# Optimization experiments

Measured on AMD Instinct MI355X. Metric: run time of the kernel, lower is better.

## Reference

```python
import jax, jax.numpy as jnp
import numpy as np

N = 50000   # nodes
E = 800000  # edges (before self loops)
F = 128     # in_dim
H = 4       # heads
C = 32      # hidden_dim per head
HC = H * C  # 128 == F
L = 3       # n_layers
G = 64      # graphs in batch
OUT = 64    # out_dim
NEG_SLOPE = 0.2


def setup_inputs() -> dict:
    key = jax.random.key(0)
    ks = jax.random.split(key, 12)
    s = 0.1
    x = jax.random.normal(ks[0], (N, F), jnp.float32)
    src = jax.random.randint(ks[1], (E,), 0, N, dtype=jnp.int32)
    dst = jax.random.randint(ks[2], (E,), 0, N, dtype=jnp.int32)
    # even split into G graphs so no graph is empty (segment_max safe)
    batch = (jnp.arange(N, dtype=jnp.int32) * G // N).astype(jnp.int32)
    Ws = jax.random.normal(ks[3], (L, HC, HC), jnp.float32) * s       # layer0 in=F=HC
    att_src = jax.random.normal(ks[4], (L, H, C), jnp.float32) * s
    att_dst = jax.random.normal(ks[5], (L, H, C), jnp.float32) * s
    conv_b = jnp.zeros((L, HC), jnp.float32)
    gate_W = jax.random.normal(ks[6], (L + 1, HC, 1), jnp.float32) * s
    gate_b = jnp.zeros((L + 1,), jnp.float32)
    lin_W = jax.random.normal(ks[7], (L + 1, HC, OUT), jnp.float32) * s
    lin_b = jnp.zeros((L + 1, OUT), jnp.float32)
    h_weights = jnp.ones((L + 1,), jnp.float32) / (L + 1)
    h0 = jax.random.normal(ks[8], (1,), jnp.float32)
    beta = jax.random.normal(ks[9], (OUT,), jnp.float32) * s
    pool_w = jnp.ones((3,), jnp.float32) / 3.0
    return dict(x=x, src=src, dst=dst, batch=batch, Ws=Ws, att_src=att_src,
                att_dst=att_dst, conv_b=conv_b, gate_W=gate_W, gate_b=gate_b,
                lin_W=lin_W, lin_b=lin_b, h_weights=h_weights, h0=h0,
                beta=beta, pool_w=pool_w)


def _seg_softmax(e, idx, n):
    # numerically stable softmax within segments
    m = jax.ops.segment_max(e, idx, num_segments=n)
    m = jnp.where(jnp.isfinite(m), m, 0.0)
    ex = jnp.exp(e - m[idx])
    s = jax.ops.segment_sum(ex, idx, num_segments=n)
    return ex / (s[idx] + 1e-16)


def _gat_layer(x, src, dst, W, a_src, a_dst, b):
    h = (x @ W).reshape(N, H, C)               # [N,H,C]
    al_s = jnp.sum(h * a_src, axis=-1)         # [N,H]
    al_d = jnp.sum(h * a_dst, axis=-1)         # [N,H]
    e = jax.nn.leaky_relu(al_s[src] + al_d[dst], NEG_SLOPE)  # [E+N,H]
    alpha = _seg_softmax(e, dst, N)            # softmax over incoming edges
    msg = h[src] * alpha[..., None]            # [E+N,H,C]
    out = jax.ops.segment_sum(msg, dst, num_segments=N)
    return out.reshape(N, HC) + b


def _pool_block(x, gw, gb, pool_w, batch, counts):
    gate = jax.nn.sigmoid(x @ gw + gb)[:, 0]          # [N]
    a = _seg_softmax(gate, batch, G)                  # per-graph attention
    p_att = jax.ops.segment_sum(a[:, None] * x, batch, num_segments=G)
    p_mean = jax.ops.segment_sum(x, batch, num_segments=G) / counts[:, None]
    p_max = jax.ops.segment_max(x, batch, num_segments=G)
    return pool_w[0] * p_att + pool_w[1] * p_mean + pool_w[2] * p_max


def reference(x, src, dst, batch, Ws, att_src, att_dst, conv_b, gate_W,
              gate_b, lin_W, lin_b, h_weights, h0, beta, pool_w):
    loops = jnp.arange(N, dtype=src.dtype)
    src_sl = jnp.concatenate([src, loops])
    dst_sl = jnp.concatenate([dst, loops])
    counts = jax.ops.segment_sum(jnp.ones((N,), x.dtype), batch, num_segments=G)
    out = jnp.zeros((G, OUT), x.dtype)
    for i in range(L):
        p = _pool_block(x, gate_W[i], gate_b[i], pool_w, batch, counts)
        out = out + h_weights[i] * (p @ lin_W[i] + lin_b[i])
        x = _gat_layer(x, src_sl, dst_sl, Ws[i], att_src[i], att_dst[i], conv_b[i])
        if i != L - 1:
            x = jax.nn.relu(x)
    p = _pool_block(x, gate_W[L], gate_b[L], pool_w, batch, counts)
    out = out + h_weights[L] * (p @ lin_W[L] + lin_b[L])
    risk_score = out @ beta + h0[0]   # [G]
    return risk_score
```

## Files before the change

kernel.cpp:

```cpp
#include <hip/hip_runtime.h>
#include <hip/hip_fp16.h>
#include <math.h>

#define N_NODES 50000
#define N_EDGES 800000
#define HC 128
#define NH 4
#define NG 64
#define NOUT 64
#define NLAYERS 3
#define POOL_CHUNKS 16
#define PREPW_BLOCKS (NLAYERS * HC * HC / 256)
#define NBKT ((N_NODES + 127) / 128)
#define PB_BLOCKS ((N_EDGES + 4095) / 4096)
#define GEMM_BLOCKS ((N_NODES + 15) / 16)
#define POOL2_BLOCKS (NG * POOL_CHUNKS / 2)
#define AGG_BLOCKS ((N_NODES + 3) / 4)
#define XT_STRIDE 136
#define ZREG_FLOATS ((NLAYERS + 1) * NG * HC * 2 + (NLAYERS + 1) * NG)
#define ZREG_BLOCKS ((ZREG_FLOATS / 4 + 255) / 256)
#define PMAX_BLOCKS ((NLAYERS + 1) * NG * HC / 4 / 256)
#define LOG2E 1.44269504f

typedef _Float16 v4h __attribute__((ext_vector_type(4)));
typedef float v4f __attribute__((ext_vector_type(4)));
typedef float v2f __attribute__((ext_vector_type(2)));

typedef unsigned char hh_t;

__device__ __forceinline__ void graph_range(int g, int* start, int* end) {
    *start = (int)(((long long)g * N_NODES + NG - 1) / NG);
    *end   = (int)(((long long)(g + 1) * N_NODES + NG - 1) / NG);
}

__device__ __forceinline__ float atomicMaxFloat(float* addr, float val) {
    if (val >= 0.f)
        return __int_as_float(atomicMax((int*)addr, __float_as_int(val)));
    else
        return __uint_as_float(atomicMin((unsigned int*)addr, __float_as_uint(val)));
}

__device__ __forceinline__ v2f hh_decode2(unsigned int packed) {
    return __builtin_amdgcn_cvt_pk_f32_fp8((int)packed, false);
}


template<bool F32>
__device__ __forceinline__ void gemm_body(
        int b, const void* xin, const _Float16* __restrict__ Wt,
        const float* __restrict__ a_src, const float* __restrict__ a_dst,
        hh_t* __restrict__ hh, float* __restrict__ al_s, float* __restrict__ al_d,
        __half* __restrict__ xh_out, const float* __restrict__ gw,
        const float* __restrict__ gbp, float* __restrict__ gate) {
    __shared__ __align__(16) _Float16 xt[16][XT_STRIDE];
    int t = threadIdx.x;
    int w = t >> 6;
    int l = t & 63;
    int n0 = b * 16;
    if constexpr (F32) {
        const float4* xg = (const float4*)((const float*)xin + (size_t)n0 * HC);
        float4 v0 = xg[t];
        float4 v1 = xg[t + 256];
        float4 gwv = ((const float4*)gw)[t & 31];
        float p0 = v0.x * gwv.x + v0.y * gwv.y + v0.z * gwv.z + v0.w * gwv.w;
        float p1 = v1.x * gwv.x + v1.y * gwv.y + v1.z * gwv.z + v1.w * gwv.w;
#pragma unroll
        for (int mk = 16; mk >= 1; mk >>= 1) {
            p0 += __shfl_xor(p0, mk);
            p1 += __shfl_xor(p1, mk);
        }
        if ((t & 31) == 0) {
            int r = t >> 5;
            float sg0 = 1.f / (1.f + __expf(-(p0 + gbp[0])));
            float sg1 = 1.f / (1.f + __expf(-(p1 + gbp[0])));
            gate[n0 + r]     = __expf(sg0);
            gate[n0 + 8 + r] = __expf(sg1);
        }
        __half2 h00 = __floats2half2_rn(v0.x, v0.y);
        __half2 h01 = __floats2half2_rn(v0.z, v0.w);
        __half2 h10 = __floats2half2_rn(v1.x, v1.y);
        __half2 h11 = __floats2half2_rn(v1.z, v1.w);
        uint2 pa, pb;
        pa.x = *(const uint*)&h00; pa.y = *(const uint*)&h01;
        pb.x = *(const uint*)&h10; pb.y = *(const uint*)&h11;
        int row = t >> 5, colh = (t & 31) * 4;
        *(uint2*)&xt[row][colh] = pa;
        *(uint2*)&xt[row + 8][colh] = pb;
        ((uint2*)xh_out)[(size_t)n0 * (HC / 4) + t]       = pa;
        ((uint2*)xh_out)[(size_t)n0 * (HC / 4) + t + 256] = pb;
    } else {
        uint4 v = ((const uint4*)((const __half*)xin + (size_t)n0 * HC))[t];
        *(uint4*)&xt[t >> 4][(t & 15) * 8] = v;
    }
    __syncthreads();
    int m = l & 15;
    int kg = (l >> 4) * 4;
    v4h a[8];
#pragma unroll
    for (int ks = 0; ks < 8; ks++)
        a[ks] = *(const v4h*)&xt[m][kg + ks * 16];
    __syncthreads();
    const _Float16* bp0 = Wt + (uint)(w * 32 + m) * HC + kg;
    const _Float16* bp1 = bp0 + 16 * HC;
    v4f acc0 = {0.f, 0.f, 0.f, 0.f}, acc1 = {0.f, 0.f, 0.f, 0.f};
#pragma unroll
    for (int ks = 0; ks < 8; ks++) {
        v4h b0 = *(const v4h*)(bp0 + ks * 16);
        v4h b1 = *(const v4h*)(bp1 + ks * 16);
        acc0 = __builtin_amdgcn_mfma_f32_16x16x16f16(a[ks], b0, acc0, 0, 0, 0);
        acc1 = __builtin_amdgcn_mfma_f32_16x16x16f16(a[ks], b1, acc1, 0, 0, 0);
    }
    int d0 = w * 32 + m;
    float as0 = a_src[d0] * LOG2E,      ad0 = a_dst[d0] * LOG2E;
    float as1 = a_src[d0 + 16] * LOG2E, ad1 = a_dst[d0 + 16] * LOG2E;
    int rloc = (l >> 4) * 4;
    unsigned char* xt8 = (unsigned char*)&xt[0][0];
#pragma unroll
    for (int r = 0; r < 4; r++) {
        int n = n0 + rloc + r;
        int q0 = __builtin_amdgcn_cvt_pk_fp8_f32(acc0[r], acc0[r], 0, false);
        int q1 = __builtin_amdgcn_cvt_pk_fp8_f32(acc1[r], acc1[r], 0, false);
        xt8[(rloc + r) * 136 + d0]      = (unsigned char)(q0 & 0xFF);
        xt8[(rloc + r) * 136 + d0 + 16] = (unsigned char)(q1 & 0xFF);
        float vs = acc0[r] * as0 + acc1[r] * as1;
        float vd = acc0[r] * ad0 + acc1[r] * ad1;
#pragma unroll
        for (int mk = 8; mk >= 1; mk >>= 1) {
            vs += __shfl_xor(vs, mk);
            vd += __shfl_xor(vd, mk);
        }
        if ((l & 15) == 0) {
            al_s[(uint)(n * NH + w)] = vs;
            al_d[(uint)(n * NH + w)] = vd;
        }
    }
    __syncthreads();
    uint2 v = *(const uint2*)&xt8[(t >> 4) * 136 + (t & 15) * 8];
    ((uint2*)hh)[(size_t)n0 * 16 + t] = v;
}

__device__ __forceinline__ void pool_body(
        int b, const __half* __restrict__ x, const float* __restrict__ gate,
        float* __restrict__ p_att, float* __restrict__ p_sum,
        float* __restrict__ p_max, float* __restrict__ wsum) {
    int c = b * 2 + (threadIdx.x >> 7);
    int g = c >> 4;
    int chunk = c & 15;
    int d = threadIdx.x & 127;
    int start, end; graph_range(g, &start, &end);
    int cnt = end - start;
    int cstart = start + (cnt * chunk) / POOL_CHUNKS;
    int cend   = start + (cnt * (chunk + 1)) / POOL_CHUNKS;
    float aat = 0.f, asu = 0.f, amx = -INFINITY, ws = 0.f;
    int n = cstart;
    for (; n + 4 <= cend; n += 4) {
        float w0 = gate[n],     w1 = gate[n + 1];
        float w2 = gate[n + 2], w3 = gate[n + 3];
        float x0 = __half2float(x[(uint)((n + 0) * HC + d)]);
        float x1 = __half2float(x[(uint)((n + 1) * HC + d)]);
        float x2 = __half2float(x[(uint)((n + 2) * HC + d)]);
        float x3 = __half2float(x[(uint)((n + 3) * HC + d)]);
        aat = fmaf(w0, x0, aat); aat = fmaf(w1, x1, aat);
        aat = fmaf(w2, x2, aat); aat = fmaf(w3, x3, aat);
        asu += (x0 + x1) + (x2 + x3);
        amx = fmaxf(amx, fmaxf(fmaxf(x0, x1), fmaxf(x2, x3)));
        ws += (w0 + w1) + (w2 + w3);
    }
    for (; n < cend; n++) {
        float w = gate[n];
        float xv = __half2float(x[(uint)(n * HC + d)]);
        aat = fmaf(w, xv, aat);
        asu += xv;
        amx = fmaxf(amx, xv);
        ws += w;
    }
    atomicAdd(&p_att[g * HC + d], aat);
    atomicAdd(&p_sum[g * HC + d], asu);
    atomicMaxFloat(&p_max[g * HC + d], amx);
    if (d == 0) atomicAdd(&wsum[g], ws);
}

__device__ __forceinline__ void scat2_body(
        int bkt, const int* __restrict__ part, const int* __restrict__ bkttot,
        int* __restrict__ rowptr, int* __restrict__ csr_src) {
    __shared__ int degs[128];
    __shared__ int curs[128];
    __shared__ int red[256];
    __shared__ int w0tot;
    int t = threadIdx.x;
    int a = 0;
    for (int i = t; i < NBKT; i += 256)
        if (i < bkt) a += bkttot[i];
    red[t] = a;
    __syncthreads();
    for (int o = 128; o > 0; o >>= 1) {
        if (t < o) red[t] += red[t + o];
        __syncthreads();
    }
    int estart = red[0];
    int eend = estart + bkttot[bkt];
    int nstart = bkt << 7;
    int nend = nstart + 128; if (nend > N_NODES) nend = N_NODES;
    int nloc = nend - nstart;
    if (t < 128) degs[t] = 0;
    __syncthreads();
    for (int e = estart + t; e < eend; e += 256)
        atomicAdd(&degs[(part[e] >> 16) & 127], 1);
    __syncthreads();
    int v = 0, inc = 0;
    if (t < 128) {
        v = degs[t];
        inc = v;
#pragma unroll
        for (int off = 1; off < 64; off <<= 1) {
            int u = __shfl_up(inc, off);
            if ((t & 63) >= off) inc += u;
        }
    }
    if (t == 63) w0tot = inc;
    __syncthreads();
    if (t < 128) {
        int excl = inc - v + ((t >= 64) ? w0tot : 0);
        int rp = estart + excl;
        curs[t] = rp;
        if (t < nloc) rowptr[nstart + t] = rp;
    }
    __syncthreads();
    for (int e = estart + t; e < eend; e += 256) {
        int p = part[e];
        int pos = atomicAdd(&curs[(p >> 16) & 127], 1);
        csr_src[pos] = p & 0xFFFF;
    }
}

__device__ __forceinline__ void agg_body(
        int b, const hh_t* __restrict__ hh, const float* __restrict__ al_s,
        const float* __restrict__ al_d, const int* __restrict__ rowptr,
        const int* __restrict__ csr_src, const float* __restrict__ conv_b,
        __half* __restrict__ xout, int do_relu,
        const float* __restrict__ gw, const float* __restrict__ gbp,
        float* __restrict__ gate) {
    int n = b * 4 + (threadIdx.x >> 6);
    if (n >= N_NODES) return;
    int l = threadIdx.x & 63;
    int head = l >> 4;
    int le = l & 15;
    float ad = al_d[(uint)(n * NH + head)];
    const unsigned short* hhp = (const unsigned short*)hh;
    float e0 = al_s[(uint)(n * NH + head)] + ad;
    e0 = fmaxf(e0, 0.2f * e0);
    float s_uni = exp2f(e0);
    v2f vself = hh_decode2(hhp[(uint)(n * 64 + l)]);
    float ax = s_uni * vself[0], ay = s_uni * vself[1];
    int jb = rowptr[n], je = rowptr[n + 1];
    float s_part = 0.f;
    for (int j = jb; j < je; j += 16) {
        int rem = je - j;
        bool act = le < rem;
        int my_s = csr_src[j + (act ? le : 0)];
        float aa = al_s[(uint)(my_s * NH + head)];
        float e = aa + ad;
        e = fmaxf(e, 0.2f * e);
        float ex = act ? exp2f(e) : 0.f;
        s_part += ex;
        int exb = __float_as_int(ex);
        unsigned int vv[16];
#pragma unroll
        for (int u = 0; u < 16; u++) {
            int ssu = __builtin_amdgcn_readlane(my_s, u);
            vv[u] = hhp[((size_t)(uint)ssu << 6) + l];
        }
#define AGG_SLOT(U) {                                                        \
            float exu = __int_as_float(                                      \
                __builtin_amdgcn_ds_swizzle(exb, 16 + 32 * (U)));            \
            v2f vf = hh_decode2(vv[U]);                                      \
            ax = fmaf(exu, vf[0], ax);                                       \
            ay = fmaf(exu, vf[1], ay);                                       \
        }
        AGG_SLOT(0)  AGG_SLOT(1)  AGG_SLOT(2)  AGG_SLOT(3)
        AGG_SLOT(4)  AGG_SLOT(5)  AGG_SLOT(6)  AGG_SLOT(7)
        AGG_SLOT(8)  AGG_SLOT(9)  AGG_SLOT(10) AGG_SLOT(11)
        AGG_SLOT(12) AGG_SLOT(13) AGG_SLOT(14) AGG_SLOT(15)
#undef AGG_SLOT
    }
    s_part += __shfl_xor(s_part, 1);
    s_part += __shfl_xor(s_part, 2);
    s_part += __shfl_xor(s_part, 4);
    s_part += __shfl_xor(s_part, 8);
    float s = s_part + s_uni;
    float inv = 1.f / (s + 1e-16f);
    float2 cb = ((const float2*)conv_b)[l];
    float r0 = fmaf(ax, inv, cb.x);
    float r1 = fmaf(ay, inv, cb.y);
    if (do_relu) { r0 = fmaxf(r0, 0.f); r1 = fmaxf(r1, 0.f); }
    ((__half2*)xout)[(uint)(n * 64 + l)] = __floats2half2_rn(r0, r1);
    float2 gwv = ((const float2*)gw)[l];
    float gv = r0 * gwv.x + r1 * gwv.y;
#pragma unroll
    for (int m = 32; m >= 1; m >>= 1) gv += __shfl_xor(gv, m);
    if (l == 0) {
        float sg = 1.f / (1.f + __expf(-(gv + gbp[0])));
        gate[n] = __expf(sg);
    }
}


__global__ __launch_bounds__(256) void k_prep(
        const float* __restrict__ Ws, _Float16* __restrict__ Wt,
        const int* __restrict__ dst, int* __restrict__ bh,
        float* __restrict__ zreg, uint* __restrict__ pmaxw,
        int* __restrict__ rowptr) {
    int b = blockIdx.x;
    int t = threadIdx.x;
    if (b == 0 && t == 0) rowptr[N_NODES] = N_EDGES;
    if (b < PREPW_BLOCKS) {
        int e = b * 256 + t;
        int layer = e >> 14; int r = e & 16383; int k = r >> 7; int d = r & 127;
        Wt[layer * 16384 + d * 128 + k] = (_Float16)Ws[layer * 16384 + k * 128 + d];
    } else if (b < PREPW_BLOCKS + PB_BLOCKS) {
        int pb = b - PREPW_BLOCKS;
        __shared__ int cnt[NBKT];
        for (int i = t; i < NBKT; i += 256) cnt[i] = 0;
        __syncthreads();
        int base = pb * 4096;
#pragma unroll
        for (int k = 0; k < 16; k++) {
            int e = base + t + 256 * k;
            if (e < N_EDGES) atomicAdd(&cnt[dst[e] >> 7], 1);
        }
        __syncthreads();
        for (int i = t; i < NBKT; i += 256) bh[i * PB_BLOCKS + pb] = cnt[i];
    } else {
        int zb = b - PREPW_BLOCKS - PB_BLOCKS;
        if (zb < ZREG_BLOCKS) {
            int i = zb * 256 + t;
            if (i < ZREG_FLOATS / 4)
                ((float4*)zreg)[i] = make_float4(0.f, 0.f, 0.f, 0.f);
        } else {
            int i = (zb - ZREG_BLOCKS) * 256 + t;
            uint4 f; f.x = f.y = f.z = f.w = 0xFFFFFFFFu;
            ((uint4*)pmaxw)[i] = f;
        }
    }
}

__global__ __launch_bounds__(256) void k_scan_bh(int* __restrict__ bh,
                                                 int* __restrict__ bkttot) {
    __shared__ int tmp[256];
    int bkt = blockIdx.x, t = threadIdx.x;
    int v = (t < PB_BLOCKS) ? bh[bkt * PB_BLOCKS + t] : 0;
    tmp[t] = v;
    __syncthreads();
    for (int off = 1; off < 256; off <<= 1) {
        int u = (t >= off) ? tmp[t - off] : 0;
        __syncthreads();
        tmp[t] += u;
        __syncthreads();
    }
    if (t < PB_BLOCKS) bh[bkt * PB_BLOCKS + t] = tmp[t] - v;
    if (t == 255) bkttot[bkt] = tmp[255];
}

__global__ __launch_bounds__(256) void k_part(
        const int* __restrict__ src, const int* __restrict__ dst,
        const int* __restrict__ bkttot, const int* __restrict__ bh,
        int* __restrict__ part) {
    __shared__ int curs[NBKT];
    __shared__ int scan[512];
    int blk = blockIdx.x, t = threadIdx.x;
    scan[t]       = (t < NBKT) ? bkttot[t] : 0;
    scan[t + 256] = (t + 256 < NBKT) ? bkttot[t + 256] : 0;
    __syncthreads();
    for (int off = 1; off < 512; off <<= 1) {
        int u0 = (t >= off) ? scan[t - off] : 0;
        int u1 = scan[t + 256 - off];
        __syncthreads();
        scan[t] += u0;
        scan[t + 256] += u1;
        __syncthreads();
    }
    for (int i = t; i < NBKT; i += 256)
        curs[i] = (i ? scan[i - 1] : 0) + bh[i * PB_BLOCKS + blk];
    __syncthreads();
    int base = blk * 4096;
#pragma unroll
    for (int k = 0; k < 16; k++) {
        int e = base + t + 256 * k;
        if (e < N_EDGES) {
            int d = dst[e];
            int pos = atomicAdd(&curs[d >> 7], 1);
            part[pos] = src[e] | ((d & 127) << 16);
        }
    }
}


__global__ __launch_bounds__(256) void k_fused_a2(
        const int* __restrict__ part, const int* __restrict__ bkttot,
        int* __restrict__ rowptr, int* __restrict__ csr_src,
        const float* __restrict__ x0, const _Float16* __restrict__ Wt,
        const float* __restrict__ a_src, const float* __restrict__ a_dst,
        hh_t* __restrict__ hh, float* __restrict__ al_s, float* __restrict__ al_d,
        __half* __restrict__ x0h, const float* __restrict__ gw,
        const float* __restrict__ gbp, float* __restrict__ gate) {
    int b = blockIdx.x;
    if (b < NBKT) {
        scat2_body(b, part, bkttot, rowptr, csr_src);
    } else {
        gemm_body<true>(b - NBKT, x0, Wt, a_src, a_dst, hh, al_s, al_d,
                        x0h, gw, gbp, gate);
    }
}

__global__ __launch_bounds__(256) void k_fused_agg(
        const hh_t* __restrict__ hh, const float* __restrict__ al_s,
        const float* __restrict__ al_d, const int* __restrict__ rowptr,
        const int* __restrict__ csr_src, const float* __restrict__ conv_b,
        __half* __restrict__ xout, int do_relu,
        const float* __restrict__ gw, const float* __restrict__ gbp,
        float* __restrict__ gate_out,
        const __half* __restrict__ xp, const float* __restrict__ gate_in,
        float* __restrict__ p_att, float* __restrict__ p_sum,
        float* __restrict__ p_max, float* __restrict__ wsum) {
    int b = blockIdx.x;
    if (b < POOL2_BLOCKS) {
        pool_body(b, xp, gate_in, p_att, p_sum, p_max, wsum);
    } else {
        agg_body(b - POOL2_BLOCKS, hh, al_s, al_d, rowptr, csr_src, conv_b,
                 xout, do_relu, gw, gbp, gate_out);
    }
}

__global__ __launch_bounds__(256) void k_gemm(
        const __half* __restrict__ x, const _Float16* __restrict__ Wt,
        const float* __restrict__ a_src, const float* __restrict__ a_dst,
        hh_t* __restrict__ hh, float* __restrict__ al_s, float* __restrict__ al_d) {
    gemm_body<false>(blockIdx.x, x, Wt, a_src, a_dst, hh, al_s, al_d,
                     nullptr, nullptr, nullptr, nullptr);
}

__global__ __launch_bounds__(256) void k_pool(
        const __half* __restrict__ x, const float* __restrict__ gate,
        float* __restrict__ p_att, float* __restrict__ p_sum,
        float* __restrict__ p_max, float* __restrict__ wsum) {
    pool_body(blockIdx.x, x, gate, p_att, p_sum, p_max, wsum);
}


__global__ __launch_bounds__(128) void k_finish(
        const float* __restrict__ p_att, const float* __restrict__ p_sum,
        const float* __restrict__ p_max, const float* __restrict__ wsum,
        const float* __restrict__ pool_w, const float* __restrict__ lin_W,
        const float* __restrict__ lin_b, const float* __restrict__ hw,
        const float* __restrict__ beta, const float* __restrict__ h0,
        float* __restrict__ out) {
    int g = blockIdx.x, t = threadIdx.x;
    __shared__ float p[NLAYERS + 1][HC];
    int start, end; graph_range(g, &start, &end);
    float cinv = 1.f / (float)(end - start);
    float pw0 = pool_w[0], pw1 = pool_w[1], pw2 = pool_w[2];
#pragma unroll
    for (int j = 0; j <= NLAYERS; j++) {
        float winv = 1.f / (wsum[j * NG + g] + 1e-16f);
        p[j][t] = pw0 * p_att[(j * NG + g) * HC + t] * winv
                + pw1 * p_sum[(j * NG + g) * HC + t] * cinv
                + pw2 * p_max[(j * NG + g) * HC + t];
    }
    __syncthreads();
    if (t < NOUT) {
        float acc = 0.f;
#pragma unroll
        for (int j = 0; j <= NLAYERS; j++) {
            float a = lin_b[j * NOUT + t];
            const float* Wj = lin_W + (size_t)j * HC * NOUT;
            for (int k = 0; k < HC; k++) a = fmaf(p[j][k], Wj[k * NOUT + t], a);
            acc = fmaf(hw[j], a, acc);
        }
        float v = acc * beta[t];
#pragma unroll
        for (int m = 32; m >= 1; m >>= 1) v += __shfl_xor(v, m);
        if (t == 0) out[g] = v + h0[0];
    }
}


extern "C" void kernel_launch(void* const* d_in, const int* in_sizes, int n_in,
                              void* d_out, int out_size, void* d_ws, size_t ws_size,
                              hipStream_t stream) {
    const float* x0       = (const float*)d_in[0];
    const int*   src      = (const int*)d_in[1];
    const int*   dst      = (const int*)d_in[2];
    const float* Ws       = (const float*)d_in[4];
    const float* att_src  = (const float*)d_in[5];
    const float* att_dst  = (const float*)d_in[6];
    const float* conv_b   = (const float*)d_in[7];
    const float* gate_W   = (const float*)d_in[8];
    const float* gate_b   = (const float*)d_in[9];
    const float* lin_W    = (const float*)d_in[10];
    const float* lin_b    = (const float*)d_in[11];
    const float* h_w      = (const float*)d_in[12];
    const float* h0       = (const float*)d_in[13];
    const float* beta     = (const float*)d_in[14];
    const float* pool_w   = (const float*)d_in[15];

    char* base = (char*)d_ws;
    size_t off = 0;
    auto carve = [&](size_t bytes) -> char* {
        char* p = base + off;
        off = (off + bytes + 255) & ~(size_t)255;
        return p;
    };
    __half*    x0h     = (__half*)carve((size_t)N_NODES * HC * 2);
    __half*    xA      = (__half*)carve((size_t)N_NODES * HC * 2);
    __half*    xB      = (__half*)carve((size_t)N_NODES * HC * 2);
    hh_t*      hh      = (hh_t*)carve((size_t)N_NODES * HC);
    _Float16*  Wt      = (_Float16*)carve((size_t)NLAYERS * HC * HC * 2);
    float*     al_s    = (float*)carve((size_t)N_NODES * NH * 4);
    float*     al_d    = (float*)carve((size_t)N_NODES * NH * 4);
    float*     gateA   = (float*)carve((size_t)N_NODES * 4);
    float*     gateB   = (float*)carve((size_t)N_NODES * 4);
    int*       rowptr  = (int*)carve((size_t)(N_NODES + 1) * 4);
    int*       csrsrc  = (int*)carve((size_t)N_EDGES * 4);
    int*       bh      = (int*)carve((size_t)NBKT * PB_BLOCKS * 4);
    int*       bkttot  = (int*)carve((size_t)NBKT * 4);
    int*       part    = (int*)carve((size_t)N_EDGES * 4);
    float*     zreg    = (float*)carve((size_t)ZREG_FLOATS * 4);
    float*     p_att   = zreg;
    float*     p_sum   = zreg + (size_t)(NLAYERS + 1) * NG * HC;
    float*     wsum    = p_sum + (size_t)(NLAYERS + 1) * NG * HC;
    float*     p_max   = (float*)carve((size_t)(NLAYERS + 1) * NG * HC * 4);

    k_prep<<<PREPW_BLOCKS + PB_BLOCKS + ZREG_BLOCKS + PMAX_BLOCKS, 256, 0, stream>>>(
        Ws, Wt, dst, bh, zreg, (uint*)p_max, rowptr);

    k_scan_bh<<<NBKT, 256, 0, stream>>>(bh, bkttot);
    k_part<<<PB_BLOCKS, 256, 0, stream>>>(src, dst, bkttot, bh, part);

    k_fused_a2<<<NBKT + GEMM_BLOCKS, 256, 0, stream>>>(
        part, bkttot, rowptr, csrsrc,
        x0, Wt, att_src, att_dst, hh, al_s, al_d,
        x0h, gate_W, gate_b, gateA);

    k_fused_agg<<<POOL2_BLOCKS + AGG_BLOCKS, 256, 0, stream>>>(
        hh, al_s, al_d, rowptr, csrsrc, conv_b,
        xA, 1, gate_W + HC, gate_b + 1, gateB,
        x0h, gateA, p_att, p_sum, p_max, wsum);

    k_gemm<<<GEMM_BLOCKS, 256, 0, stream>>>(
        xA, Wt + (size_t)1 * HC * HC, att_src + HC, att_dst + HC,
        hh, al_s, al_d);

    k_fused_agg<<<POOL2_BLOCKS + AGG_BLOCKS, 256, 0, stream>>>(
        hh, al_s, al_d, rowptr, csrsrc, conv_b + HC,
        xB, 1, gate_W + 2 * HC, gate_b + 2, gateA,
        xA, gateB,
        p_att + (size_t)1 * NG * HC, p_sum + (size_t)1 * NG * HC,
        p_max + (size_t)1 * NG * HC, wsum + 1 * NG);

    k_gemm<<<GEMM_BLOCKS, 256, 0, stream>>>(
        xB, Wt + (size_t)2 * HC * HC, att_src + 2 * HC, att_dst + 2 * HC,
        hh, al_s, al_d);

    k_fused_agg<<<POOL2_BLOCKS + AGG_BLOCKS, 256, 0, stream>>>(
        hh, al_s, al_d, rowptr, csrsrc, conv_b + 2 * HC,
        xA, 0, gate_W + 3 * HC, gate_b + 3, gateB,
        xB, gateA,
        p_att + (size_t)2 * NG * HC, p_sum + (size_t)2 * NG * HC,
        p_max + (size_t)2 * NG * HC, wsum + 2 * NG);

    k_pool<<<POOL2_BLOCKS, 256, 0, stream>>>(
        xA, gateB,
        p_att + (size_t)3 * NG * HC, p_sum + (size_t)3 * NG * HC,
        p_max + (size_t)3 * NG * HC, wsum + 3 * NG);

    k_finish<<<NG, 128, 0, stream>>>(p_att, p_sum, p_max, wsum, pool_w,
                                     lin_W, lin_b, h_w, beta, h0, (float*)d_out);
}
```

Before: 252.6 us.

## Pool layer-0 input from fp32 directly and fuse pooling into GEMM kernels

Removes the fp16 copy of the input features written by the first GEMM; layer-0 pooling now reads the original fp32 input directly. Pooling for layers 1 and 2 moves out of the aggregation kernels and into the following GEMM kernels, so the aggregation kernels run alone. This cuts one full-size fp16 write and changes which work shares a launch, but layer-0 pooling now reads twice as many bytes as before.

```diff
diff --git a/kernel.cpp b/kernel.cpp
--- a/kernel.cpp
+++ b/kernel.cpp
@@ -50,8 +50,8 @@
         int b, const void* xin, const _Float16* __restrict__ Wt,
         const float* __restrict__ a_src, const float* __restrict__ a_dst,
         hh_t* __restrict__ hh, float* __restrict__ al_s, float* __restrict__ al_d,
-        __half* __restrict__ xh_out, const float* __restrict__ gw,
-        const float* __restrict__ gbp, float* __restrict__ gate) {
+        const float* __restrict__ gw, const float* __restrict__ gbp,
+        float* __restrict__ gate) {
     __shared__ __align__(16) _Float16 xt[16][XT_STRIDE];
     int t = threadIdx.x;
     int w = t >> 6;
@@ -86,8 +86,6 @@
         int row = t >> 5, colh = (t & 31) * 4;
         *(uint2*)&xt[row][colh] = pa;
         *(uint2*)&xt[row + 8][colh] = pb;
-        ((uint2*)xh_out)[(size_t)n0 * (HC / 4) + t]       = pa;
-        ((uint2*)xh_out)[(size_t)n0 * (HC / 4) + t + 256] = pb;
     } else {
         uint4 v = ((const uint4*)((const __half*)xin + (size_t)n0 * HC))[t];
         *(uint4*)&xt[t >> 4][(t & 15) * 8] = v;
@@ -139,8 +137,9 @@
     ((uint2*)hh)[(size_t)n0 * 16 + t] = v;
 }
 
+template<typename T>
 __device__ __forceinline__ void pool_body(
-        int b, const __half* __restrict__ x, const float* __restrict__ gate,
+        int b, const T* __restrict__ x, const float* __restrict__ gate,
         float* __restrict__ p_att, float* __restrict__ p_sum,
         float* __restrict__ p_max, float* __restrict__ wsum) {
     int c = b * 2 + (threadIdx.x >> 7);
@@ -152,14 +151,16 @@
     int cstart = start + (cnt * chunk) / POOL_CHUNKS;
     int cend   = start + (cnt * (chunk + 1)) / POOL_CHUNKS;
     float aat = 0.f, asu = 0.f, amx = -INFINITY, ws = 0.f;
+    auto ld = [&](int n) -> float {
+        if constexpr (sizeof(T) == 4) return ((const float*)x)[(uint)(n * HC + d)];
+        else return __half2float(((const __half*)x)[(uint)(n * HC + d)]);
+    };
     int n = cstart;
     for (; n + 4 <= cend; n += 4) {
         float w0 = gate[n],     w1 = gate[n + 1];
         float w2 = gate[n + 2], w3 = gate[n + 3];
-        float x0 = __half2float(x[(uint)((n + 0) * HC + d)]);
-        float x1 = __half2float(x[(uint)((n + 1) * HC + d)]);
-        float x2 = __half2float(x[(uint)((n + 2) * HC + d)]);
-        float x3 = __half2float(x[(uint)((n + 3) * HC + d)]);
+        float x0 = ld(n),     x1 = ld(n + 1);
+        float x2 = ld(n + 2), x3 = ld(n + 3);
         aat = fmaf(w0, x0, aat); aat = fmaf(w1, x1, aat);
         aat = fmaf(w2, x2, aat); aat = fmaf(w3, x3, aat);
         asu += (x0 + x1) + (x2 + x3);
@@ -168,7 +169,7 @@
     }
     for (; n < cend; n++) {
         float w = gate[n];
-        float xv = __half2float(x[(uint)(n * HC + d)]);
+        float xv = ld(n);
         aat = fmaf(w, xv, aat);
         asu += xv;
         amx = fmaxf(amx, xv);
@@ -401,49 +402,68 @@
         const float* __restrict__ x0, const _Float16* __restrict__ Wt,
         const float* __restrict__ a_src, const float* __restrict__ a_dst,
         hh_t* __restrict__ hh, float* __restrict__ al_s, float* __restrict__ al_d,
-        __half* __restrict__ x0h, const float* __restrict__ gw,
-        const float* __restrict__ gbp, float* __restrict__ gate) {
+        const float* __restrict__ gw, const float* __restrict__ gbp,
+        float* __restrict__ gate) {
     int b = blockIdx.x;
     if (b < NBKT) {
         scat2_body(b, part, bkttot, rowptr, csr_src);
     } else {
         gemm_body<true>(b - NBKT, x0, Wt, a_src, a_dst, hh, al_s, al_d,
-                        x0h, gw, gbp, gate);
-    }
-}
-
-__global__ __launch_bounds__(256) void k_fused_agg(
+                        gw, gbp, gate);
+    }
+}
+
+__global__ __launch_bounds__(256) void k_fused_agg0(
         const hh_t* __restrict__ hh, const float* __restrict__ al_s,
         const float* __restrict__ al_d, const int* __restrict__ rowptr,
         const int* __restrict__ csr_src, const float* __restrict__ conv_b,
         __half* __restrict__ xout, int do_relu,
         const float* __restrict__ gw, const float* __restrict__ gbp,
         float* __restrict__ gate_out,
-        const __half* __restrict__ xp, const float* __restrict__ gate_in,
+        const float* __restrict__ xp, const float* __restrict__ gate_in,
         float* __restrict__ p_att, float* __restrict__ p_sum,
         float* __restrict__ p_max, float* __restrict__ wsum) {
     int b = blockIdx.x;
     if (b < POOL2_BLOCKS) {
-        pool_body(b, xp, gate_in, p_att, p_sum, p_max, wsum);
+        pool_body<float>(b, xp, gate_in, p_att, p_sum, p_max, wsum);
     } else {
         agg_body(b - POOL2_BLOCKS, hh, al_s, al_d, rowptr, csr_src, conv_b,
                  xout, do_relu, gw, gbp, gate_out);
     }
 }
 
-__global__ __launch_bounds__(256) void k_gemm(
+__global__ __launch_bounds__(256) void k_fused_b(
         const __half* __restrict__ x, const _Float16* __restrict__ Wt,
         const float* __restrict__ a_src, const float* __restrict__ a_dst,
-        hh_t* __restrict__ hh, float* __restrict__ al_s, float* __restrict__ al_d) {
-    gemm_body<false>(blockIdx.x, x, Wt, a_src, a_dst, hh, al_s, al_d,
-                     nullptr, nullptr, nullptr, nullptr);
+        hh_t* __restrict__ hh, float* __restrict__ al_s, float* __restrict__ al_d,
+        const float* __restrict__ gate,
+        float* __restrict__ p_att, float* __restrict__ p_sum,
+        float* __restrict__ p_max, float* __restrict__ wsum) {
+    int b = blockIdx.x;
+    if (b < GEMM_BLOCKS) {
+        gemm_body<false>(b, x, Wt, a_src, a_dst, hh, al_s, al_d,
+                         nullptr, nullptr, nullptr);
+    } else {
+        pool_body<__half>(b - GEMM_BLOCKS, x, gate, p_att, p_sum, p_max, wsum);
+    }
+}
+
+__global__ __launch_bounds__(256) void k_agg(
+        const hh_t* __restrict__ hh, const float* __restrict__ al_s,
+        const float* __restrict__ al_d, const int* __restrict__ rowptr,
+        const int* __restrict__ csr_src, const float* __restrict__ conv_b,
+        __half* __restrict__ xout, int do_relu,
+        const float* __restrict__ gw, const float* __restrict__ gbp,
+        float* __restrict__ gate) {
+    agg_body(blockIdx.x, hh, al_s, al_d, rowptr, csr_src, conv_b,
+             xout, do_relu, gw, gbp, gate);
 }
 
 __global__ __launch_bounds__(256) void k_pool(
         const __half* __restrict__ x, const float* __restrict__ gate,
         float* __restrict__ p_att, float* __restrict__ p_sum,
         float* __restrict__ p_max, float* __restrict__ wsum) {
-    pool_body(blockIdx.x, x, gate, p_att, p_sum, p_max, wsum);
+    pool_body<__half>(blockIdx.x, x, gate, p_att, p_sum, p_max, wsum);
 }
 
 
@@ -510,7 +530,6 @@
         off = (off + bytes + 255) & ~(size_t)255;
         return p;
     };
-    __half*    x0h     = (__half*)carve((size_t)N_NODES * HC * 2);
     __half*    xA      = (__half*)carve((size_t)N_NODES * HC * 2);
     __half*    xB      = (__half*)carve((size_t)N_NODES * HC * 2);
     hh_t*      hh      = (hh_t*)carve((size_t)N_NODES * HC);
@@ -539,34 +558,32 @@
     k_fused_a2<<<NBKT + GEMM_BLOCKS, 256, 0, stream>>>(
         part, bkttot, rowptr, csrsrc,
         x0, Wt, att_src, att_dst, hh, al_s, al_d,
-        x0h, gate_W, gate_b, gateA);
-
-    k_fused_agg<<<POOL2_BLOCKS + AGG_BLOCKS, 256, 0, stream>>>(
+        gate_W, gate_b, gateA);
+
+    k_fused_agg0<<<POOL2_BLOCKS + AGG_BLOCKS, 256, 0, stream>>>(
         hh, al_s, al_d, rowptr, csrsrc, conv_b,
         xA, 1, gate_W + HC, gate_b + 1, gateB,
-        x0h, gateA, p_att, p_sum, p_max, wsum);
-
-    k_gemm<<<GEMM_BLOCKS, 256, 0, stream>>>(
+        x0, gateA, p_att, p_sum, p_max, wsum);
+
+    k_fused_b<<<GEMM_BLOCKS + POOL2_BLOCKS, 256, 0, stream>>>(
         xA, Wt + (size_t)1 * HC * HC, att_src + HC, att_dst + HC,
-        hh, al_s, al_d);
-
-    k_fused_agg<<<POOL2_BLOCKS + AGG_BLOCKS, 256, 0, stream>>>(
-        hh, al_s, al_d, rowptr, csrsrc, conv_b + HC,
-        xB, 1, gate_W + 2 * HC, gate_b + 2, gateA,
-        xA, gateB,
+        hh, al_s, al_d, gateB,
         p_att + (size_t)1 * NG * HC, p_sum + (size_t)1 * NG * HC,
         p_max + (size_t)1 * NG * HC, wsum + 1 * NG);
 
-    k_gemm<<<GEMM_BLOCKS, 256, 0, stream>>>(
+    k_agg<<<AGG_BLOCKS, 256, 0, stream>>>(
+        hh, al_s, al_d, rowptr, csrsrc, conv_b + HC,
+        xB, 1, gate_W + 2 * HC, gate_b + 2, gateA);
+
+    k_fused_b<<<GEMM_BLOCKS + POOL2_BLOCKS, 256, 0, stream>>>(
         xB, Wt + (size_t)2 * HC * HC, att_src + 2 * HC, att_dst + 2 * HC,
-        hh, al_s, al_d);
-
-    k_fused_agg<<<POOL2_BLOCKS + AGG_BLOCKS, 256, 0, stream>>>(
-        hh, al_s, al_d, rowptr, csrsrc, conv_b + 2 * HC,
-        xA, 0, gate_W + 3 * HC, gate_b + 3, gateB,
-        xB, gateA,
+        hh, al_s, al_d, gateA,
         p_att + (size_t)2 * NG * HC, p_sum + (size_t)2 * NG * HC,
         p_max + (size_t)2 * NG * HC, wsum + 2 * NG);
+
+    k_agg<<<AGG_BLOCKS, 256, 0, stream>>>(
+        hh, al_s, al_d, rowptr, csrsrc, conv_b + 2 * HC,
+        xA, 0, gate_W + 3 * HC, gate_b + 3, gateB);
 
     k_pool<<<POOL2_BLOCKS, 256, 0, stream>>>(
         xA, gateB,
```

Result: faster. 245.3 us (-2.9%).
